# Performance work log

Measured on AMD Instinct MI355X. Metric: run time of the kernel, lower is better.

## Reference

```python
import jax, jax.numpy as jnp
import numpy as np

B, G = 256, 24
N = B * G
D_IN, HEADS, D_HEAD = 128, 8, 64  # out_channels = in_channels//2 = 64, concat=False
EFF = HEADS * D_HEAD
EPS = 1e-5
SCALE = float(np.sqrt(D_HEAD))

def _gelu(x):
    return jax.nn.gelu(x, approximate=False)

def _pff(x, w1, b1, w2, b2):
    # PositionwiseFeedForward, dropout=0 (eval)
    return _gelu(x @ w1.T + b1) @ w2.T + b2

def _graph_norm_global(x, w, b, ms):
    # GraphNorm called without batch -> single graph over all N nodes
    mean = jnp.mean(x, axis=0, keepdims=True)
    out = x - mean * ms
    var = jnp.mean(out * out, axis=0, keepdims=True)
    return w * out / jnp.sqrt(var + EPS) + b

def _graph_norm(x, w, b, ms, batch, nseg):
    cnt = jax.ops.segment_sum(jnp.ones((x.shape[0],), x.dtype), batch, nseg)[:, None]
    mean = jax.ops.segment_sum(x, batch, nseg) / cnt
    out = x - mean[batch] * ms
    var = jax.ops.segment_sum(out * out, batch, nseg) / cnt
    return w * out / jnp.sqrt(var + EPS)[batch] + b

def _segment_softmax(logits, seg, nseg):
    m = jax.ops.segment_max(logits, seg, num_segments=nseg)
    e = jnp.exp(logits - m[seg])
    s = jax.ops.segment_sum(e, seg, num_segments=nseg)
    return e / (s[seg] + 1e-16)

def _attn_conv(x, edge_index, p):
    (nq_w, nq_b, nq_ms, wq, bq, wk, bk, wv, bv,
     no_w, no_b, no_ms, o_w1, o_b1, o_w2, o_b2) = p
    n = x.shape[0]
    xin = x
    xn = _graph_norm_global(x, nq_w, nq_b, nq_ms)
    q = (xn @ wq.T + bq).reshape(n, HEADS, D_HEAD)
    k = (xn @ wk.T + bk).reshape(n, HEADS, D_HEAD)
    v = (xn @ wv.T + bv).reshape(n, HEADS, D_HEAD)
    loops = jnp.arange(n, dtype=edge_index.dtype)  # add_self_loops appends
    src = jnp.concatenate([edge_index[0], loops])
    dst = jnp.concatenate([edge_index[1], loops])
    qk = jnp.sum(q[dst] * k[src], axis=-1) / SCALE          # [E', H]
    alpha = _segment_softmax(qk, dst, n)                     # segment softmax over dst
    aggr = jax.ops.segment_sum(v[src] * alpha[:, :, None], dst, num_segments=n)  # [N,H,Dh]
    aggr = aggr.mean(axis=1)                                 # concat=False: head mean -> [N,64]
    init = xin.reshape(n, D_IN // D_HEAD, D_HEAD).sum(axis=1)  # sum-fold 128 -> 64 residual
    h = aggr + init
    hn = _graph_norm_global(h, no_w, no_b, no_ms)
    return h + _pff(hn, o_w1, o_b1, o_w2, o_b2)


def setup_inputs() -> dict:
    key = jax.random.key(0)
    ks = jax.random.split(key, 12)
    # block-dense edges: fully connected within each set, no self loops
    a = np.arange(G)
    ii, jj = np.meshgrid(a, a, indexing='ij')
    m = ii != jj
    dst_l, src_l = ii[m], jj[m]
    offs = (np.arange(B) * G)[:, None]
    src = (src_l[None, :] + offs).reshape(-1)
    dst = (dst_l[None, :] + offs).reshape(-1)
    edge_index = jnp.asarray(np.stack([src, dst]), dtype=jnp.int64)
    batch = jnp.asarray(np.repeat(np.arange(B), G), dtype=jnp.int64)
    ptr = jnp.asarray(np.arange(B + 1) * G, dtype=jnp.int64)
    x = jax.random.normal(ks[0], (N, D_IN), jnp.float32)
    def lin(k, o, i):
        return jax.random.normal(k, (o, i), jnp.float32) * (1.0 / np.sqrt(i))
    d = dict(x=x, edge_index=edge_index, ptr=ptr, batch=batch)
    d.update(nq_w=jnp.ones((D_IN,)), nq_b=jnp.zeros((D_IN,)), nq_ms=jnp.ones((D_IN,)))
    d.update(wq=lin(ks[1], EFF, D_IN), bq=jnp.zeros((EFF,)),
             wk=lin(ks[2], EFF, D_IN), bk=jnp.zeros((EFF,)),
             wv=lin(ks[3], EFF, D_IN), bv=jnp.zeros((EFF,)))
    d.update(no_w=jnp.ones((D_HEAD,)), no_b=jnp.zeros((D_HEAD,)), no_ms=jnp.ones((D_HEAD,)))
    d.update(o_w1=lin(ks[4], D_HEAD, D_HEAD), o_b1=jnp.zeros((D_HEAD,)),
             o_w2=lin(ks[5], D_HEAD, D_HEAD), o_b2=jnp.zeros((D_HEAD,)))
    d.update(pn_w=jnp.ones((D_HEAD,)), pn_b=jnp.zeros((D_HEAD,)), pn_ms=jnp.ones((D_HEAD,)))
    d.update(p_w1=lin(ks[6], D_HEAD, D_HEAD), p_b1=jnp.zeros((D_HEAD,)),
             p_w2=lin(ks[7], 1, D_HEAD), p_b2=jnp.zeros((1,)))
    return d


def reference(x, edge_index, ptr, batch,
              nq_w, nq_b, nq_ms, wq, bq, wk, bk, wv, bv,
              no_w, no_b, no_ms, o_w1, o_b1, o_w2, o_b2,
              pn_w, pn_b, pn_ms, p_w1, p_b1, p_w2, p_b2):
    nseg = ptr.shape[0] - 1
    h = _attn_conv(x, edge_index,
                   (nq_w, nq_b, nq_ms, wq, bq, wk, bk, wv, bv,
                    no_w, no_b, no_ms, o_w1, o_b1, o_w2, o_b2))   # [N,64]
    hn = _graph_norm(h, pn_w, pn_b, pn_ms, batch, nseg)
    score = _pff(hn, p_w1, p_b1, p_w2, p_b2)                       # [N,1]
    w = _segment_softmax(score[:, 0], batch, nseg)[:, None]        # per-set softmax
    return jax.ops.segment_sum(x * w, batch, num_segments=nseg)    # [B, 128]
```

## Files before the change

kernel.cpp:

```cpp
#include <hip/hip_runtime.h>
#include <stdint.h>


#define N_NODES 6144
#define GSIZE 24
#define NGRAPH 256
#define DIN 128
#define DH 64
#define EFF 512
#define EPSN 1e-5f

typedef __attribute__((ext_vector_type(8))) __bf16 bf16x8;
typedef __attribute__((ext_vector_type(4))) float f32x4;
union U16B { uint4 u; bf16x8 v; unsigned short s[8]; };

__device__ inline float bf2f(unsigned short u){ return __uint_as_float(((unsigned)u)<<16); }
__device__ inline unsigned short f2bf(float f){
  unsigned u = __float_as_uint(f);
  u += 0x7fff + ((u>>16)&1);
  return (unsigned short)(u>>16);
}
__device__ inline float gelu_exact(float x){ return 0.5f*x*(1.0f+erff(x*0.70710678118654752f)); }

#define XP    0
#define HP    49152
#define WT1   81920
#define WT2   86016
#define PWT1  90112
#define FBo   94208
#define WCVT_BYTE  385024
#define HCOMB_BYTE 778240

__global__ __launch_bounds__(256)
void k_pre(const float* __restrict__ x,
           const float* __restrict__ o_w1, const float* __restrict__ o_w2,
           const float* __restrict__ p_w1,
           const float* __restrict__ o_b1, const float* __restrict__ o_b2,
           const float* __restrict__ p_b1, const float* __restrict__ p_w2,
           const float* __restrict__ p_b2,
           const float* __restrict__ wq, const float* __restrict__ wk,
           const float* __restrict__ wv,
           float* __restrict__ wsf){
  int t = threadIdx.x;
  int bi = blockIdx.x;
  if(bi < 192){
    int c = t & 127, h = t >> 7;
    float s = 0.f, q = 0.f;
    #pragma unroll
    for(int r = 0; r < 16; ++r){
      float v = x[(size_t)(bi*32 + h + 2*r)*DIN + c];
      s += v; q += v*v;
    }
    __shared__ float sm[256], sm2[256];
    sm[t] = s; sm2[t] = q;
    __syncthreads();
    if(t < 128){
      wsf[XP + bi*256 + t]       = sm[t] + sm[t+128];
      wsf[XP + bi*256 + 128 + t] = sm2[t] + sm2[t+128];
    }
    return;
  }
  if(bi < 195){
    const float* src; float* dst;
    if(bi == 192){ src = o_w1; dst = wsf + WT1; }
    else if(bi == 193){ src = o_w2; dst = wsf + WT2; }
    else { src = p_w1; dst = wsf + PWT1; }
    for(int p = t; p < DH*DH; p += 256){
      int r = p >> 6, c = p & 63;
      dst[c*DH + r] = src[p];
    }
    if(bi == 192){
      float* fb = wsf + FBo;
      if(t < 64){
        fb[t]       = o_b1[t];
        fb[64 + t]  = o_b2[t];
        fb[128 + t] = p_b1[t];
        fb[192 + t] = p_w2[t];
      }
      if(t == 0) fb[256] = p_b2[0];
    }
    return;
  }
  int j = bi - 195;
  int mat = j >> 2, seg = j & 3;
  const float* src = (mat==0) ? wq : (mat==1) ? wk : wv;
  unsigned short* dst = (unsigned short*)((char*)wsf + WCVT_BYTE)
                        + (size_t)mat*EFF*DIN + seg*16384;
  const float* sp = src + seg*16384;
  for(int e = t*8; e < 16384; e += 2048){
    float4 a = *(const float4*)(sp + e);
    float4 b = *(const float4*)(sp + e + 4);
    U16B o;
    o.s[0]=f2bf(a.x); o.s[1]=f2bf(a.y); o.s[2]=f2bf(a.z); o.s[3]=f2bf(a.w);
    o.s[4]=f2bf(b.x); o.s[5]=f2bf(b.y); o.s[6]=f2bf(b.z); o.s[7]=f2bf(b.w);
    *(uint4*)(dst + e) = o.u;
  }
}

__global__ __launch_bounds__(512)
void k_fused(const float* __restrict__ x,
             const float* __restrict__ bq, const float* __restrict__ bk,
             const float* __restrict__ bv,
             const float* __restrict__ nq_w, const float* __restrict__ nq_b,
             const float* __restrict__ nq_ms,
             float* __restrict__ ws, float* __restrict__ hcomb){
  __shared__ __align__(16) char arena[52224];
  float (*hv)[68] = (float(*)[68])(arena);
  float* A1 = (float*)(arena + 6528);
  float* C1 = (float*)(arena + 7040);
  float (*qs)[GSIZE][68] = (float(*)[GSIZE][68])(arena + 7552);
  float (*ks)[GSIZE][68] = (float(*)[GSIZE][68])(arena + 20608);
  float (*vs)[GSIZE][68] = (float(*)[GSIZE][68])(arena + 33664);
  float (*S)[GSIZE][28]  = (float(*)[GSIZE][28])(arena + 46720);
  float* redA = (float*)(arena + 7552);
  float* redB = (float*)(arena + 11648);

  int t = threadIdx.x, g = blockIdx.x, base = g * GSIZE;
  const unsigned short* wcvt = (const unsigned short*)((const char*)ws + WCVT_BYTE);

  {
    int c = t & 127, grp = t >> 7;
    float s = 0.f, q = 0.f;
    for(int p = grp*48; p < grp*48 + 48; ++p){
      s += ws[XP + p*256 + c];
      q += ws[XP + p*256 + 128 + c];
    }
    redA[t] = s; redB[t] = q;
  }
  __syncthreads();
  if(t < 128){
    float s = redA[t] + redA[t+128] + redA[t+256] + redA[t+384];
    float q = redB[t] + redB[t+128] + redB[t+256] + redB[t+384];
    float mean = s * (1.0f / N_NODES);
    float ex2  = q * (1.0f / N_NODES);
    float cm   = mean * nq_ms[t];
    float var  = ex2 - 2.f*cm*mean + cm*cm;
    float rstd = rsqrtf(var + EPSN);
    float a    = nq_w[t] * rstd;
    A1[t] = a; C1[t] = nq_b[t] - a*cm;
  }
  __syncthreads();

  int pipe = t >> 8, t2 = t & 255;
  int wv4 = (t >> 6) & 3, lane = t & 63, m = lane & 15, quad = lane >> 4;
  int mt = wv4 & 1, cth = wv4 >> 1;
  int node = mt*16 + m;
  int xrow = base + node; if(xrow > N_NODES-1) xrow = N_NODES-1;

  bf16x8 xfr[4];
  #pragma unroll
  for(int kk = 0; kk < 4; kk++){
    int k0 = kk*32 + quad*8;
    float4 a = *(const float4*)(x + (size_t)xrow*DIN + k0);
    float4 b = *(const float4*)(x + (size_t)xrow*DIN + k0 + 4);
    U16B u;
    u.s[0] = f2bf(a.x*A1[k0+0] + C1[k0+0]);
    u.s[1] = f2bf(a.y*A1[k0+1] + C1[k0+1]);
    u.s[2] = f2bf(a.z*A1[k0+2] + C1[k0+2]);
    u.s[3] = f2bf(a.w*A1[k0+3] + C1[k0+3]);
    u.s[4] = f2bf(b.x*A1[k0+4] + C1[k0+4]);
    u.s[5] = f2bf(b.y*A1[k0+5] + C1[k0+5]);
    u.s[6] = f2bf(b.z*A1[k0+6] + C1[k0+6]);
    u.s[7] = f2bf(b.w*A1[k0+7] + C1[k0+7]);
    xfr[kk] = u.v;
  }

  uint4 wbuf[6][4];
  float4 bb[6];
  {
    int hh = pipe;
    #pragma unroll
    for(int task = 0; task < 6; ++task){
      int tk = cth*6 + task;
      int mat = tk >> 2, ctm = tk & 3;
      const unsigned short* wp = wcvt + (size_t)mat*EFF*DIN
                               + (size_t)(hh*64 + ctm*16 + m)*DIN + quad*8;
      #pragma unroll
      for(int kk = 0; kk < 4; kk++) wbuf[task][kk] = *(const uint4*)(wp + kk*32);
      const float* bias = (mat==0) ? bq : (mat==1) ? bk : bv;
      bb[task] = *(const float4*)(bias + hh*64 + ctm*16 + quad*4);
    }
  }

  f32x4 a0 = {0.f,0.f,0.f,0.f}, a1 = {0.f,0.f,0.f,0.f};

  for(int iter = 0; iter < 4; ++iter){
    __syncthreads();
    #pragma unroll
    for(int task = 0; task < 6; ++task){
      int tk = cth*6 + task;
      int mat = tk >> 2, ctm = tk & 3;
      f32x4 acc = {0.f,0.f,0.f,0.f};
      #pragma unroll
      for(int kk = 0; kk < 4; kk++){
        U16B w8; w8.u = wbuf[task][kk];
        acc = __builtin_amdgcn_mfma_f32_16x16x32_bf16(w8.v, xfr[kk], acc, 0, 0, 0);
      }
      float (*tile)[68] = (mat==0) ? qs[pipe] : (mat==1) ? ks[pipe] : vs[pipe];
      if(mt == 0 || m < 8){
        int d0 = ctm*16 + quad*4;
        tile[node][d0+0] = acc[0] + bb[task].x;
        tile[node][d0+1] = acc[1] + bb[task].y;
        tile[node][d0+2] = acc[2] + bb[task].z;
        tile[node][d0+3] = acc[3] + bb[task].w;
      }
    }
    __syncthreads();
    if(iter < 3){
      int hh = (iter+1)*2 + pipe;
      #pragma unroll
      for(int task = 0; task < 6; ++task){
        int tk = cth*6 + task;
        int mat = tk >> 2, ctm = tk & 3;
        const unsigned short* wp = wcvt + (size_t)mat*EFF*DIN
                                 + (size_t)(hh*64 + ctm*16 + m)*DIN + quad*8;
        #pragma unroll
        for(int kk = 0; kk < 4; kk++) wbuf[task][kk] = *(const uint4*)(wp + kk*32);
        const float* bias = (mat==0) ? bq : (mat==1) ? bk : bv;
        bb[task] = *(const float4*)(bias + hh*64 + ctm*16 + quad*4);
      }
    }
    if(t2 < 192){
      int row = t2 >> 3, sl = t2 & 7;
      const float4* qi = (const float4*)qs[pipe][row];
      const float4* k0p = (const float4*)ks[pipe][sl*3];
      const float4* k1p = (const float4*)ks[pipe][sl*3+1];
      const float4* k2p = (const float4*)ks[pipe][sl*3+2];
      float s0 = 0.f, s1 = 0.f, s2 = 0.f;
      #pragma unroll
      for(int d = 0; d < 16; ++d){
        float4 qv = qi[d];
        float4 ka = k0p[d], kb = k1p[d], kc = k2p[d];
        s0 += qv.x*ka.x + qv.y*ka.y + qv.z*ka.z + qv.w*ka.w;
        s1 += qv.x*kb.x + qv.y*kb.y + qv.z*kb.z + qv.w*kb.w;
        s2 += qv.x*kc.x + qv.y*kc.y + qv.z*kc.z + qv.w*kc.w;
      }
      s0 *= 0.125f; s1 *= 0.125f; s2 *= 0.125f;
      float m0 = fmaxf(fmaxf(s0, s1), s2);
      #pragma unroll
      for(int o = 1; o < 8; o <<= 1) m0 = fmaxf(m0, __shfl_xor(m0, o, 8));
      float e0 = __expf(s0-m0), e1 = __expf(s1-m0), e2 = __expf(s2-m0);
      float su = e0 + e1 + e2;
      #pragma unroll
      for(int o = 1; o < 8; o <<= 1) su += __shfl_xor(su, o, 8);
      float inv = 1.0f / (su + 1e-16f);
      S[pipe][row][sl*3]   = e0*inv;
      S[pipe][row][sl*3+1] = e1*inv;
      S[pipe][row][sl*3+2] = e2*inv;
    }
    __syncthreads();
    {
      int p = t2;
      if(p < 384){
        int i = p >> 4, dq = p & 15;
        #pragma unroll 8
        for(int j = 0; j < GSIZE; ++j){
          float w = S[pipe][i][j];
          float4 v = *(const float4*)&vs[pipe][j][dq*4];
          a0.x += w*v.x; a0.y += w*v.y; a0.z += w*v.z; a0.w += w*v.w;
        }
      }
      p = t2 + 256;
      if(p < 384){
        int i = p >> 4, dq = p & 15;
        #pragma unroll 8
        for(int j = 0; j < GSIZE; ++j){
          float w = S[pipe][i][j];
          float4 v = *(const float4*)&vs[pipe][j][dq*4];
          a1.x += w*v.x; a1.y += w*v.y; a1.z += w*v.z; a1.w += w*v.w;
        }
      }
    }
  }
  __syncthreads();
  if(pipe == 1){
    int p = t2;
    if(p < 384){
      int i = p >> 4, dq = p & 15;
      float4 o; o.x = a0.x*0.125f; o.y = a0.y*0.125f; o.z = a0.z*0.125f; o.w = a0.w*0.125f;
      *(float4*)&hv[i][dq*4] = o;
    }
    p = t2 + 256;
    if(p < 384){
      int i = p >> 4, dq = p & 15;
      float4 o; o.x = a1.x*0.125f; o.y = a1.y*0.125f; o.z = a1.z*0.125f; o.w = a1.w*0.125f;
      *(float4*)&hv[i][dq*4] = o;
    }
  }
  __syncthreads();
  if(pipe == 0){
    #pragma unroll
    for(int slot = 0; slot < 2; ++slot){
      int p = t2 + slot*256;
      if(p < 384){
        int i = p >> 4, dq = p & 15;
        f32x4 a = slot ? a1 : a0;
        float4 hp = *(const float4*)&hv[i][dq*4];
        const float* xr = x + (size_t)(base+i)*DIN + dq*4;
        float4 r1 = *(const float4*)xr;
        float4 r2 = *(const float4*)(xr + 64);
        float4 o;
        o.x = a.x*0.125f + hp.x + r1.x + r2.x;
        o.y = a.y*0.125f + hp.y + r1.y + r2.y;
        o.z = a.z*0.125f + hp.z + r1.z + r2.z;
        o.w = a.w*0.125f + hp.w + r1.w + r2.w;
        *(float4*)&hv[i][dq*4] = o;
        *(float4*)(hcomb + (size_t)(base+i)*DH + dq*4) = o;
      }
    }
  }
  __syncthreads();
  if(t < 64){
    float s1 = 0.f, s2 = 0.f;
    #pragma unroll
    for(int i = 0; i < GSIZE; ++i){ float v = hv[i][t]; s1 += v; s2 += v*v; }
    ws[HP + g*128 + t]      = s1;
    ws[HP + g*128 + 64 + t] = s2;
  }
}

__global__ __launch_bounds__(256)
void k_final(const float* __restrict__ x,
             const float* __restrict__ hbuf, const float* __restrict__ ws,
             const float* __restrict__ no_w, const float* __restrict__ no_b,
             const float* __restrict__ no_ms,
             const float* __restrict__ pn_w, const float* __restrict__ pn_b,
             const float* __restrict__ pn_ms,
             float* __restrict__ out){
  const float* wt1  = ws + WT1;
  const float* wt2  = ws + WT2;
  const float* pwt1 = ws + PWT1;
  const float* fb   = ws + FBo;

  __shared__ float hs[GSIZE][DH+1];
  __shared__ float hn[GSIZE][DH+1];
  __shared__ float ts[GSIZE][DH+1];
  __shared__ float A2[DH], C2[DH];
  __shared__ float a3[DH], c3[DH];
  __shared__ float scores[GSIZE], wsm[GSIZE];
  __shared__ float redA[256], redB[256];

  int t = threadIdx.x;
  int base = blockIdx.x * GSIZE;

  {
    int c = t & 63, grp = t >> 6;
    float s1 = 0.f, s2 = 0.f;
    for(int p = grp; p < NGRAPH; p += 4){
      s1 += ws[HP + p*128 + c];
      s2 += ws[HP + p*128 + 64 + c];
    }
    redA[t] = s1; redB[t] = s2;
  }
  __syncthreads();
  if(t < DH){
    float s1 = redA[t] + redA[t+64] + redA[t+128] + redA[t+192];
    float s2 = redB[t] + redB[t+64] + redB[t+128] + redB[t+192];
    float mean = s1 * (1.0f / N_NODES);
    float ex2  = s2 * (1.0f / N_NODES);
    float cm   = mean * no_ms[t];
    float var  = ex2 - 2.f*cm*mean + cm*cm;
    float rstd = rsqrtf(var + EPSN);
    float a    = no_w[t] * rstd;
    A2[t] = a; C2[t] = no_b[t] - a*cm;
  }
  __syncthreads();
  for(int p = t; p < GSIZE*DH; p += 256){
    int i = p >> 6, d = p & 63;
    float hvv = hbuf[(size_t)(base+i)*DH + d];
    hs[i][d] = hvv;
    hn[i][d] = A2[d]*hvv + C2[d];
  }
  __syncthreads();
  for(int p = t; p < GSIZE*DH; p += 256){
    int i = p >> 6, c = p & 63;
    float s = fb[c];
    #pragma unroll
    for(int k = 0; k < DH; k++) s += hn[i][k] * wt1[k*DH + c];
    ts[i][c] = gelu_exact(s);
  }
  __syncthreads();
  for(int p = t; p < GSIZE*DH; p += 256){
    int i = p >> 6, c = p & 63;
    float s = fb[64 + c];
    #pragma unroll
    for(int k = 0; k < DH; k++) s += ts[i][k] * wt2[k*DH + c];
    hs[i][c] = hs[i][c] + s;
  }
  __syncthreads();
  if(t < DH){
    float s1 = 0.f, s2 = 0.f;
    for(int i = 0; i < GSIZE; i++){ float v = hs[i][t]; s1 += v; s2 += v*v; }
    float mean = s1 * (1.0f / GSIZE);
    float ex2  = s2 * (1.0f / GSIZE);
    float cm   = mean * pn_ms[t];
    float var  = ex2 - 2.f*cm*mean + cm*cm;
    float rstd = rsqrtf(var + EPSN);
    float a    = pn_w[t] * rstd;
    a3[t] = a; c3[t] = pn_b[t] - a*cm;
  }
  __syncthreads();
  for(int p = t; p < GSIZE*DH; p += 256){
    int i = p >> 6, d = p & 63;
    hn[i][d] = a3[d]*hs[i][d] + c3[d];
  }
  __syncthreads();
  for(int p = t; p < GSIZE*DH; p += 256){
    int i = p >> 6, c = p & 63;
    float s = fb[128 + c];
    #pragma unroll
    for(int k = 0; k < DH; k++) s += hn[i][k] * pwt1[k*DH + c];
    ts[i][c] = gelu_exact(s);
  }
  __syncthreads();
  if(t < GSIZE){
    float s = fb[256];
    for(int c = 0; c < DH; c++) s += ts[t][c] * fb[192 + c];
    scores[t] = s;
  }
  __syncthreads();
  if(t < GSIZE){
    float mx = -1e30f;
    for(int j = 0; j < GSIZE; j++) mx = fmaxf(mx, scores[j]);
    float sum = 0.f;
    for(int j = 0; j < GSIZE; j++) sum += __expf(scores[j] - mx);
    wsm[t] = __expf(scores[t] - mx) / (sum + 1e-16f);
  }
  __syncthreads();
  if(t < DIN){
    float s = 0.f;
    #pragma unroll 8
    for(int i = 0; i < GSIZE; i++) s += wsm[i] * x[(size_t)(base+i)*DIN + t];
    out[(size_t)blockIdx.x*DIN + t] = s;
  }
}

extern "C" void kernel_launch(void* const* d_in, const int* in_sizes, int n_in,
                              void* d_out, int out_size, void* d_ws, size_t ws_size,
                              hipStream_t stream){
  (void)in_sizes; (void)n_in; (void)out_size; (void)ws_size;
  const float* x    = (const float*)d_in[0];
  const float* nq_w = (const float*)d_in[4];
  const float* nq_b = (const float*)d_in[5];
  const float* nq_ms= (const float*)d_in[6];
  const float* wq   = (const float*)d_in[7];
  const float* bq   = (const float*)d_in[8];
  const float* wk   = (const float*)d_in[9];
  const float* bk   = (const float*)d_in[10];
  const float* wv   = (const float*)d_in[11];
  const float* bv   = (const float*)d_in[12];
  const float* no_w = (const float*)d_in[13];
  const float* no_b = (const float*)d_in[14];
  const float* no_ms= (const float*)d_in[15];
  const float* o_w1 = (const float*)d_in[16];
  const float* o_b1 = (const float*)d_in[17];
  const float* o_w2 = (const float*)d_in[18];
  const float* o_b2 = (const float*)d_in[19];
  const float* pn_w = (const float*)d_in[20];
  const float* pn_b = (const float*)d_in[21];
  const float* pn_ms= (const float*)d_in[22];
  const float* p_w1 = (const float*)d_in[23];
  const float* p_b1 = (const float*)d_in[24];
  const float* p_w2 = (const float*)d_in[25];
  const float* p_b2 = (const float*)d_in[26];

  float* ws = (float*)d_ws;
  float* hcomb = (float*)((char*)d_ws + HCOMB_BYTE);

  k_pre<<<207, 256, 0, stream>>>(x, o_w1, o_w2, p_w1, o_b1, o_b2, p_b1, p_w2, p_b2,
                                 wq, wk, wv, ws);
  k_fused<<<NGRAPH, 512, 0, stream>>>(x, bq, bk, bv, nq_w, nq_b, nq_ms, ws, hcomb);
  k_final<<<NGRAPH, 256, 0, stream>>>(x, hcomb, ws, no_w, no_b, no_ms,
                                      pn_w, pn_b, pn_ms, (float*)d_out);
}
```

Before: 182.6 us.

## Split fused attention kernel into stats, tiled QKV GEMM, and attention kernels

Result: slower. 202.4 us (+10.9%).

```diff
diff --git a/kernel.cpp b/kernel.cpp
--- a/kernel.cpp
+++ b/kernel.cpp
@@ -28,8 +28,10 @@
 #define WT2   86016
 #define PWT1  90112
 #define FBo   94208
+#define AC    94720
 #define WCVT_BYTE  385024
 #define HCOMB_BYTE 778240
+#define QKV_BYTE   2359296
 
 __global__ __launch_bounds__(256)
 void k_pre(const float* __restrict__ x,
@@ -98,216 +100,212 @@
 }
 
 __global__ __launch_bounds__(512)
-void k_fused(const float* __restrict__ x,
-             const float* __restrict__ bq, const float* __restrict__ bk,
-             const float* __restrict__ bv,
-             const float* __restrict__ nq_w, const float* __restrict__ nq_b,
-             const float* __restrict__ nq_ms,
-             float* __restrict__ ws, float* __restrict__ hcomb){
-  __shared__ __align__(16) char arena[52224];
-  float (*hv)[68] = (float(*)[68])(arena);
-  float* A1 = (float*)(arena + 6528);
-  float* C1 = (float*)(arena + 7040);
-  float (*qs)[GSIZE][68] = (float(*)[GSIZE][68])(arena + 7552);
-  float (*ks)[GSIZE][68] = (float(*)[GSIZE][68])(arena + 20608);
-  float (*vs)[GSIZE][68] = (float(*)[GSIZE][68])(arena + 33664);
-  float (*S)[GSIZE][28]  = (float(*)[GSIZE][28])(arena + 46720);
-  float* redA = (float*)(arena + 7552);
-  float* redB = (float*)(arena + 11648);
-
-  int t = threadIdx.x, g = blockIdx.x, base = g * GSIZE;
-  const unsigned short* wcvt = (const unsigned short*)((const char*)ws + WCVT_BYTE);
-
-  {
-    int c = t & 127, grp = t >> 7;
-    float s = 0.f, q = 0.f;
-    for(int p = grp*48; p < grp*48 + 48; ++p){
-      s += ws[XP + p*256 + c];
-      q += ws[XP + p*256 + 128 + c];
-    }
-    redA[t] = s; redB[t] = q;
-  }
+void k_stats(const float* __restrict__ nq_w, const float* __restrict__ nq_b,
+             const float* __restrict__ nq_ms, float* __restrict__ ws){
+  __shared__ float redA[512], redB[512];
+  int t = threadIdx.x;
+  int c = t & 127, grp = t >> 7;
+  float s = 0.f, q = 0.f;
+  for(int p = grp*48; p < grp*48 + 48; ++p){
+    s += ws[XP + p*256 + c];
+    q += ws[XP + p*256 + 128 + c];
+  }
+  redA[t] = s; redB[t] = q;
   __syncthreads();
   if(t < 128){
-    float s = redA[t] + redA[t+128] + redA[t+256] + redA[t+384];
-    float q = redB[t] + redB[t+128] + redB[t+256] + redB[t+384];
-    float mean = s * (1.0f / N_NODES);
-    float ex2  = q * (1.0f / N_NODES);
+    float s1 = redA[t] + redA[t+128] + redA[t+256] + redA[t+384];
+    float q1 = redB[t] + redB[t+128] + redB[t+256] + redB[t+384];
+    float mean = s1 * (1.0f / N_NODES);
+    float ex2  = q1 * (1.0f / N_NODES);
     float cm   = mean * nq_ms[t];
     float var  = ex2 - 2.f*cm*mean + cm*cm;
     float rstd = rsqrtf(var + EPSN);
     float a    = nq_w[t] * rstd;
-    A1[t] = a; C1[t] = nq_b[t] - a*cm;
-  }
-  __syncthreads();
-
-  int pipe = t >> 8, t2 = t & 255;
-  int wv4 = (t >> 6) & 3, lane = t & 63, m = lane & 15, quad = lane >> 4;
-  int mt = wv4 & 1, cth = wv4 >> 1;
-  int node = mt*16 + m;
-  int xrow = base + node; if(xrow > N_NODES-1) xrow = N_NODES-1;
-
-  bf16x8 xfr[4];
+    ws[AC + t]       = a;
+    ws[AC + 128 + t] = nq_b[t] - a*cm;
+  }
+}
+
+__global__ __launch_bounds__(256)
+void k_qkv(const float* __restrict__ x,
+           const float* __restrict__ bq, const float* __restrict__ bk,
+           const float* __restrict__ bv,
+           const float* __restrict__ ws, float* __restrict__ qkv){
+  __shared__ __align__(16) char lds[65536];
+  char* Alds = lds;
+  char* Blds = lds + 32768;
+  int t = threadIdx.x;
+  int mt = blockIdx.x / 12, nt = blockIdx.x % 12;
+  int mat = nt >> 2, obase = (nt & 3) * 128;
+  const float* A1c = ws + AC;
+  const unsigned short* wsrc = (const unsigned short*)((const char*)ws + WCVT_BYTE)
+                               + (size_t)mat*EFF*DIN + (size_t)obase*DIN;
+  {
+    int kf = (t & 31) * 4;
+    float4 a4 = *(const float4*)(A1c + kf);
+    float4 c4 = *(const float4*)(A1c + 128 + kf);
+    #pragma unroll
+    for(int it = 0; it < 16; ++it){
+      int row = it*8 + (t >> 5);
+      float4 v = *(const float4*)(x + (size_t)(mt*128 + row)*DIN + kf);
+      ushort4 us;
+      us.x = f2bf(v.x*a4.x + c4.x);
+      us.y = f2bf(v.y*a4.y + c4.y);
+      us.z = f2bf(v.z*a4.z + c4.z);
+      us.w = f2bf(v.w*a4.w + c4.w);
+      *(ushort4*)(Alds + ((row*256 + kf*2) ^ ((row & 7) << 4))) = us;
+    }
+  }
+  {
+    int kb = (t & 15) * 16;
+    #pragma unroll
+    for(int it = 0; it < 8; ++it){
+      int row = it*16 + (t >> 4);
+      uint4 w = *(const uint4*)((const char*)wsrc + row*256 + kb);
+      *(uint4*)(Blds + ((row*256 + kb) ^ ((row & 7) << 4))) = w;
+    }
+  }
+  __syncthreads();
+  int wv4 = t >> 6, l = t & 63;
+  int wr = wv4 >> 1, wc = wv4 & 1;
+  int lm = l & 15, lq = l >> 4;
+  f32x4 acc[4][4];
   #pragma unroll
-  for(int kk = 0; kk < 4; kk++){
-    int k0 = kk*32 + quad*8;
-    float4 a = *(const float4*)(x + (size_t)xrow*DIN + k0);
-    float4 b = *(const float4*)(x + (size_t)xrow*DIN + k0 + 4);
-    U16B u;
-    u.s[0] = f2bf(a.x*A1[k0+0] + C1[k0+0]);
-    u.s[1] = f2bf(a.y*A1[k0+1] + C1[k0+1]);
-    u.s[2] = f2bf(a.z*A1[k0+2] + C1[k0+2]);
-    u.s[3] = f2bf(a.w*A1[k0+3] + C1[k0+3]);
-    u.s[4] = f2bf(b.x*A1[k0+4] + C1[k0+4]);
-    u.s[5] = f2bf(b.y*A1[k0+5] + C1[k0+5]);
-    u.s[6] = f2bf(b.z*A1[k0+6] + C1[k0+6]);
-    u.s[7] = f2bf(b.w*A1[k0+7] + C1[k0+7]);
-    xfr[kk] = u.v;
-  }
-
-  uint4 wbuf[6][4];
-  float4 bb[6];
+  for(int m = 0; m < 4; ++m)
+    #pragma unroll
+    for(int n = 0; n < 4; ++n) acc[m][n] = (f32x4){0.f,0.f,0.f,0.f};
+  #pragma unroll
+  for(int kk = 0; kk < 4; ++kk){
+    int kbyte = kk*64 + lq*16;
+    bf16x8 af[4], bf[4];
+    #pragma unroll
+    for(int m = 0; m < 4; ++m){
+      int row = wr*64 + m*16 + lm;
+      af[m] = *(const bf16x8*)(Alds + ((row*256 + kbyte) ^ ((row & 7) << 4)));
+    }
+    #pragma unroll
+    for(int n = 0; n < 4; ++n){
+      int row = wc*64 + n*16 + lm;
+      bf[n] = *(const bf16x8*)(Blds + ((row*256 + kbyte) ^ ((row & 7) << 4)));
+    }
+    #pragma unroll
+    for(int m = 0; m < 4; ++m)
+      #pragma unroll
+      for(int n = 0; n < 4; ++n)
+        acc[m][n] = __builtin_amdgcn_mfma_f32_16x16x32_bf16(af[m], bf[n], acc[m][n], 0, 0, 0);
+  }
+  const float* bias = (mat==0) ? bq : (mat==1) ? bk : bv;
+  #pragma unroll
+  for(int n = 0; n < 4; ++n){
+    float bn = bias[obase + wc*64 + n*16 + lm];
+    int gcol = nt*128 + wc*64 + n*16 + lm;
+    #pragma unroll
+    for(int m = 0; m < 4; ++m){
+      int grow0 = mt*128 + wr*64 + m*16 + lq*4;
+      #pragma unroll
+      for(int r = 0; r < 4; ++r)
+        qkv[(size_t)(grow0 + r)*1536 + gcol] = acc[m][n][r] + bn;
+    }
+  }
+}
+
+__global__ __launch_bounds__(512)
+void k_attn(const float* __restrict__ x, const float* __restrict__ qkv,
+            float* __restrict__ ws, float* __restrict__ hcomb){
+  __shared__ __align__(16) float ST[8][GSIZE][28];
+  __shared__ __align__(16) float hv[GSIZE][68];
+  int t = threadIdx.x, g = blockIdx.x, base = g * GSIZE;
+  int h = t >> 6, l = t & 63;
+
+  for(int i = t; i < GSIZE*68; i += 512) ((float*)hv)[i] = 0.f;
+
+  int r0 = 3*(l >> 3), j0 = 3*(l & 7);
+  const float* qp = qkv + (size_t)(base + r0)*1536 + h*64;
+  const float* kp = qkv + (size_t)(base + j0)*1536 + 512 + h*64;
+  float s00=0.f,s01=0.f,s02=0.f,s10=0.f,s11=0.f,s12=0.f,s20=0.f,s21=0.f,s22=0.f;
+  #pragma unroll
+  for(int d4 = 0; d4 < 16; ++d4){
+    float4 q0 = *(const float4*)(qp + d4*4);
+    float4 q1 = *(const float4*)(qp + 1536 + d4*4);
+    float4 q2 = *(const float4*)(qp + 3072 + d4*4);
+    float4 k0 = *(const float4*)(kp + d4*4);
+    float4 k1 = *(const float4*)(kp + 1536 + d4*4);
+    float4 k2 = *(const float4*)(kp + 3072 + d4*4);
+    s00 += q0.x*k0.x + q0.y*k0.y + q0.z*k0.z + q0.w*k0.w;
+    s01 += q0.x*k1.x + q0.y*k1.y + q0.z*k1.z + q0.w*k1.w;
+    s02 += q0.x*k2.x + q0.y*k2.y + q0.z*k2.z + q0.w*k2.w;
+    s10 += q1.x*k0.x + q1.y*k0.y + q1.z*k0.z + q1.w*k0.w;
+    s11 += q1.x*k1.x + q1.y*k1.y + q1.z*k1.z + q1.w*k1.w;
+    s12 += q1.x*k2.x + q1.y*k2.y + q1.z*k2.z + q1.w*k2.w;
+    s20 += q2.x*k0.x + q2.y*k0.y + q2.z*k0.z + q2.w*k0.w;
+    s21 += q2.x*k1.x + q2.y*k1.y + q2.z*k1.z + q2.w*k1.w;
+    s22 += q2.x*k2.x + q2.y*k2.y + q2.z*k2.z + q2.w*k2.w;
+  }
   {
-    int hh = pipe;
-    #pragma unroll
-    for(int task = 0; task < 6; ++task){
-      int tk = cth*6 + task;
-      int mat = tk >> 2, ctm = tk & 3;
-      const unsigned short* wp = wcvt + (size_t)mat*EFF*DIN
-                               + (size_t)(hh*64 + ctm*16 + m)*DIN + quad*8;
+    float a0, a1, a2, m0, su, inv;
+    a0 = s00*0.125f; a1 = s01*0.125f; a2 = s02*0.125f;
+    m0 = fmaxf(fmaxf(a0, a1), a2);
+    #pragma unroll
+    for(int o = 1; o < 8; o <<= 1) m0 = fmaxf(m0, __shfl_xor(m0, o, 8));
+    a0 = __expf(a0-m0); a1 = __expf(a1-m0); a2 = __expf(a2-m0);
+    su = a0 + a1 + a2;
+    #pragma unroll
+    for(int o = 1; o < 8; o <<= 1) su += __shfl_xor(su, o, 8);
+    inv = 1.0f/(su + 1e-16f);
+    ST[h][j0+0][r0+0] = a0*inv; ST[h][j0+1][r0+0] = a1*inv; ST[h][j0+2][r0+0] = a2*inv;
+    a0 = s10*0.125f; a1 = s11*0.125f; a2 = s12*0.125f;
+    m0 = fmaxf(fmaxf(a0, a1), a2);
+    #pragma unroll
+    for(int o = 1; o < 8; o <<= 1) m0 = fmaxf(m0, __shfl_xor(m0, o, 8));
+    a0 = __expf(a0-m0); a1 = __expf(a1-m0); a2 = __expf(a2-m0);
+    su = a0 + a1 + a2;
+    #pragma unroll
+    for(int o = 1; o < 8; o <<= 1) su += __shfl_xor(su, o, 8);
+    inv = 1.0f/(su + 1e-16f);
+    ST[h][j0+0][r0+1] = a0*inv; ST[h][j0+1][r0+1] = a1*inv; ST[h][j0+2][r0+1] = a2*inv;
+    a0 = s20*0.125f; a1 = s21*0.125f; a2 = s22*0.125f;
+    m0 = fmaxf(fmaxf(a0, a1), a2);
+    #pragma unroll
+    for(int o = 1; o < 8; o <<= 1) m0 = fmaxf(m0, __shfl_xor(m0, o, 8));
+    a0 = __expf(a0-m0); a1 = __expf(a1-m0); a2 = __expf(a2-m0);
+    su = a0 + a1 + a2;
+    #pragma unroll
+    for(int o = 1; o < 8; o <<= 1) su += __shfl_xor(su, o, 8);
+    inv = 1.0f/(su + 1e-16f);
+    ST[h][j0+0][r0+2] = a0*inv; ST[h][j0+1][r0+2] = a1*inv; ST[h][j0+2][r0+2] = a2*inv;
+  }
+  __syncthreads();
+
+  {
+    float o24[GSIZE];
+    #pragma unroll
+    for(int r = 0; r < GSIZE; ++r) o24[r] = 0.f;
+    const float* vp = qkv + (size_t)base*1536 + 1024 + h*64 + l;
+    #pragma unroll
+    for(int j = 0; j < GSIZE; ++j){
+      float v = vp[(size_t)j*1536];
       #pragma unroll
-      for(int kk = 0; kk < 4; kk++) wbuf[task][kk] = *(const uint4*)(wp + kk*32);
-      const float* bias = (mat==0) ? bq : (mat==1) ? bk : bv;
-      bb[task] = *(const float4*)(bias + hh*64 + ctm*16 + quad*4);
-    }
-  }
-
-  f32x4 a0 = {0.f,0.f,0.f,0.f}, a1 = {0.f,0.f,0.f,0.f};
-
-  for(int iter = 0; iter < 4; ++iter){
-    __syncthreads();
-    #pragma unroll
-    for(int task = 0; task < 6; ++task){
-      int tk = cth*6 + task;
-      int mat = tk >> 2, ctm = tk & 3;
-      f32x4 acc = {0.f,0.f,0.f,0.f};
-      #pragma unroll
-      for(int kk = 0; kk < 4; kk++){
-        U16B w8; w8.u = wbuf[task][kk];
-        acc = __builtin_amdgcn_mfma_f32_16x16x32_bf16(w8.v, xfr[kk], acc, 0, 0, 0);
+      for(int rq = 0; rq < 6; ++rq){
+        float4 p4 = *(const float4*)&ST[h][j][rq*4];
+        o24[rq*4+0] = fmaf(p4.x, v, o24[rq*4+0]);
+        o24[rq*4+1] = fmaf(p4.y, v, o24[rq*4+1]);
+        o24[rq*4+2] = fmaf(p4.z, v, o24[rq*4+2]);
+        o24[rq*4+3] = fmaf(p4.w, v, o24[rq*4+3]);
       }
-      float (*tile)[68] = (mat==0) ? qs[pipe] : (mat==1) ? ks[pipe] : vs[pipe];
-      if(mt == 0 || m < 8){
-        int d0 = ctm*16 + quad*4;
-        tile[node][d0+0] = acc[0] + bb[task].x;
-        tile[node][d0+1] = acc[1] + bb[task].y;
-        tile[node][d0+2] = acc[2] + bb[task].z;
-        tile[node][d0+3] = acc[3] + bb[task].w;
-      }
-    }
-    __syncthreads();
-    if(iter < 3){
-      int hh = (iter+1)*2 + pipe;
-      #pragma unroll
-      for(int task = 0; task < 6; ++task){
-        int tk = cth*6 + task;
-        int mat = tk >> 2, ctm = tk & 3;
-        const unsigned short* wp = wcvt + (size_t)mat*EFF*DIN
-                                 + (size_t)(hh*64 + ctm*16 + m)*DIN + quad*8;
-        #pragma unroll
-        for(int kk = 0; kk < 4; kk++) wbuf[task][kk] = *(const uint4*)(wp + kk*32);
-        const float* bias = (mat==0) ? bq : (mat==1) ? bk : bv;
-        bb[task] = *(const float4*)(bias + hh*64 + ctm*16 + quad*4);
-      }
-    }
-    if(t2 < 192){
-      int row = t2 >> 3, sl = t2 & 7;
-      const float4* qi = (const float4*)qs[pipe][row];
-      const float4* k0p = (const float4*)ks[pipe][sl*3];
-      const float4* k1p = (const float4*)ks[pipe][sl*3+1];
-      const float4* k2p = (const float4*)ks[pipe][sl*3+2];
-      float s0 = 0.f, s1 = 0.f, s2 = 0.f;
-      #pragma unroll
-      for(int d = 0; d < 16; ++d){
-        float4 qv = qi[d];
-        float4 ka = k0p[d], kb = k1p[d], kc = k2p[d];
-        s0 += qv.x*ka.x + qv.y*ka.y + qv.z*ka.z + qv.w*ka.w;
-        s1 += qv.x*kb.x + qv.y*kb.y + qv.z*kb.z + qv.w*kb.w;
-        s2 += qv.x*kc.x + qv.y*kc.y + qv.z*kc.z + qv.w*kc.w;
-      }
-      s0 *= 0.125f; s1 *= 0.125f; s2 *= 0.125f;
-      float m0 = fmaxf(fmaxf(s0, s1), s2);
-      #pragma unroll
-      for(int o = 1; o < 8; o <<= 1) m0 = fmaxf(m0, __shfl_xor(m0, o, 8));
-      float e0 = __expf(s0-m0), e1 = __expf(s1-m0), e2 = __expf(s2-m0);
-      float su = e0 + e1 + e2;
-      #pragma unroll
-      for(int o = 1; o < 8; o <<= 1) su += __shfl_xor(su, o, 8);
-      float inv = 1.0f / (su + 1e-16f);
-      S[pipe][row][sl*3]   = e0*inv;
-      S[pipe][row][sl*3+1] = e1*inv;
-      S[pipe][row][sl*3+2] = e2*inv;
-    }
-    __syncthreads();
-    {
-      int p = t2;
-      if(p < 384){
-        int i = p >> 4, dq = p & 15;
-        #pragma unroll 8
-        for(int j = 0; j < GSIZE; ++j){
-          float w = S[pipe][i][j];
-          float4 v = *(const float4*)&vs[pipe][j][dq*4];
-          a0.x += w*v.x; a0.y += w*v.y; a0.z += w*v.z; a0.w += w*v.w;
-        }
-      }
-      p = t2 + 256;
-      if(p < 384){
-        int i = p >> 4, dq = p & 15;
-        #pragma unroll 8
-        for(int j = 0; j < GSIZE; ++j){
-          float w = S[pipe][i][j];
-          float4 v = *(const float4*)&vs[pipe][j][dq*4];
-          a1.x += w*v.x; a1.y += w*v.y; a1.z += w*v.z; a1.w += w*v.w;
-        }
-      }
-    }
-  }
-  __syncthreads();
-  if(pipe == 1){
-    int p = t2;
-    if(p < 384){
-      int i = p >> 4, dq = p & 15;
-      float4 o; o.x = a0.x*0.125f; o.y = a0.y*0.125f; o.z = a0.z*0.125f; o.w = a0.w*0.125f;
-      *(float4*)&hv[i][dq*4] = o;
-    }
-    p = t2 + 256;
-    if(p < 384){
-      int i = p >> 4, dq = p & 15;
-      float4 o; o.x = a1.x*0.125f; o.y = a1.y*0.125f; o.z = a1.z*0.125f; o.w = a1.w*0.125f;
-      *(float4*)&hv[i][dq*4] = o;
-    }
-  }
-  __syncthreads();
-  if(pipe == 0){
-    #pragma unroll
-    for(int slot = 0; slot < 2; ++slot){
-      int p = t2 + slot*256;
-      if(p < 384){
-        int i = p >> 4, dq = p & 15;
-        f32x4 a = slot ? a1 : a0;
-        float4 hp = *(const float4*)&hv[i][dq*4];
-        const float* xr = x + (size_t)(base+i)*DIN + dq*4;
-        float4 r1 = *(const float4*)xr;
-        float4 r2 = *(const float4*)(xr + 64);
-        float4 o;
-        o.x = a.x*0.125f + hp.x + r1.x + r2.x;
-        o.y = a.y*0.125f + hp.y + r1.y + r2.y;
-        o.z = a.z*0.125f + hp.z + r1.z + r2.z;
-        o.w = a.w*0.125f + hp.w + r1.w + r2.w;
-        *(float4*)&hv[i][dq*4] = o;
-        *(float4*)(hcomb + (size_t)(base+i)*DH + dq*4) = o;
-      }
-    }
+    }
+    #pragma unroll
+    for(int r = 0; r < GSIZE; ++r) atomicAdd(&hv[r][l], o24[r]);
+  }
+  __syncthreads();
+
+  #pragma unroll
+  for(int sl = 0; sl < 3; ++sl){
+    int idx = t + sl*512;
+    int r = idx >> 6, d = idx & 63;
+    const float* xr = x + (size_t)(base + r)*DIN;
+    float hval = hv[r][d]*0.125f + xr[d] + xr[64 + d];
+    hcomb[(size_t)(base + r)*DH + d] = hval;
+    hv[r][d] = hval;
   }
   __syncthreads();
   if(t < 64){
@@ -464,12 +462,15 @@
   const float* p_w2 = (const float*)d_in[25];
   const float* p_b2 = (const float*)d_in[26];
 
-  float* ws = (float*)d_ws;
+  float* ws    = (float*)d_ws;
   float* hcomb = (float*)((char*)d_ws + HCOMB_BYTE);
+  float* qkvb  = (float*)((char*)d_ws + QKV_BYTE);
 
   k_pre<<<207, 256, 0, stream>>>(x, o_w1, o_w2, p_w1, o_b1, o_b2, p_b1, p_w2, p_b2,
                                  wq, wk, wv, ws);
-  k_fused<<<NGRAPH, 512, 0, stream>>>(x, bq, bk, bv, nq_w, nq_b, nq_ms, ws, hcomb);
+  k_stats<<<1, 512, 0, stream>>>(nq_w, nq_b, nq_ms, ws);
+  k_qkv<<<576, 256, 0, stream>>>(x, bq, bk, bv, ws, qkvb);
+  k_attn<<<NGRAPH, 512, 0, stream>>>(x, qkvb, ws, hcomb);
   k_final<<<NGRAPH, 256, 0, stream>>>(x, hcomb, ws, no_w, no_b, no_ms,
                                       pn_w, pn_b, pn_ms, (float*)d_out);
 }
```
